# Optimization experiments

Hardware: AMD Instinct MI355X
Metric: run time of the kernel (lower is better)

## Reference

```python
import jax, jax.numpy as jnp
import numpy as np

N_NODES = 50000
N_EDGES = 1600000
IN_DIM, HIDDEN, OUT_DIM = 128, 128, 64


def setup_inputs() -> dict:
    key = jax.random.key(0)
    ks = jax.random.split(key, 8)
    x = jax.random.normal(ks[0], (N_NODES, IN_DIM), dtype=jnp.float32)
    edge_index = jax.random.randint(ks[1], (2, N_EDGES), 0, N_NODES, dtype=jnp.int64)
    # SAGEConv params: lin_l applied to aggregated neighbors (with bias),
    # lin_r applied to root/self features (no bias) -- PyG defaults.
    def lin_init(k, fan_in, fan_out):
        bound = 1.0 / np.sqrt(fan_in)
        return jax.random.uniform(k, (fan_in, fan_out), jnp.float32, -bound, bound)
    W1_l = lin_init(ks[2], IN_DIM, HIDDEN)
    W1_r = lin_init(ks[3], IN_DIM, HIDDEN)
    b1 = jnp.zeros((HIDDEN,), jnp.float32)
    W2_l = lin_init(ks[4], HIDDEN, OUT_DIM)
    W2_r = lin_init(ks[5], HIDDEN, OUT_DIM)
    b2 = jnp.zeros((OUT_DIM,), jnp.float32)
    return {"x": x, "edge_index": edge_index, "W1_l": W1_l, "W1_r": W1_r,
            "b1": b1, "W2_l": W2_l, "W2_r": W2_r, "b2": b2}


def _sage_conv(h, src, dst, n_nodes, W_l, W_r, b):
    # gather messages from source nodes, mean-aggregate at destinations
    msg = h[src]                                              # [E, D]
    agg_sum = jax.ops.segment_sum(msg, dst, num_segments=n_nodes)
    deg = jax.ops.segment_sum(jnp.ones((src.shape[0],), h.dtype), dst,
                              num_segments=n_nodes)
    agg_mean = agg_sum / jnp.maximum(deg, 1.0)[:, None]       # [N, D]
    return agg_mean @ W_l + h @ W_r + b


def reference(x, edge_index, W1_l, W1_r, b1, W2_l, W2_r, b2):
    n = x.shape[0]
    src, dst = edge_index[0], edge_index[1]
    h = jax.nn.relu(_sage_conv(x, src, dst, n, W1_l, W1_r, b1))
    return _sage_conv(h, src, dst, n, W2_l, W2_r, b2)
```

## Files before the change

kernel.cpp:

```cpp
#include <hip/hip_runtime.h>

#define NN 50000
#define NE 1600000
#define BSTRIDE 96
#define C_BKT 196
#define P1_BLKS 512
#define P1_CHUNK 3125
#define CAP 56
#define XCVT_BLKS 1563
#define WCVT_BLKS 48
#define PP_PREP (XCVT_BLKS + WCVT_BLKS)

typedef __bf16 bf16x8 __attribute__((ext_vector_type(8)));
typedef float  f32x4  __attribute__((ext_vector_type(4)));
typedef float  f32x2  __attribute__((ext_vector_type(2)));

__device__ __forceinline__ float bfLo(uint u) { union { uint i; float f; } v; v.i = u << 16; return v.f; }
__device__ __forceinline__ float bfHi(uint u) { union { uint i; float f; } v; v.i = u & 0xffff0000u; return v.f; }
__device__ __forceinline__ float bf1(ushort s) { union { uint i; float f; } v; v.i = (uint)s << 16; return v.f; }
__device__ __forceinline__ ushort f2bf(float f) {
    union { float f; uint i; } v; v.f = f;
    uint r = v.i + 0x7fffu + ((v.i >> 16) & 1u);
    return (ushort)(r >> 16);
}
__device__ __forceinline__ uint pack2(float a, float b) {
    return (uint)f2bf(a) | ((uint)f2bf(b) << 16);
}
__device__ __forceinline__ bf16x8 load8(const ushort* p) {
    union { uint4 u; bf16x8 b; } v; v.u = *(const uint4*)p; return v.b;
}

#define ACC8(u) { a0 += bfLo(u.x); a1 += bfHi(u.x); a2 += bfLo(u.y); a3 += bfHi(u.y); \
                  a4 += bfLo(u.z); a5 += bfHi(u.z); a6 += bfLo(u.w); a7 += bfHi(u.w); }

#define CVA(u, o) { f32x2 p0 = __builtin_amdgcn_cvt_pk_f32_fp8((int)(u), 0); \
                    f32x2 p1 = __builtin_amdgcn_cvt_pk_f32_fp8((int)(u), 1); \
                    a[(o)+0] += p0.x; a[(o)+1] += p0.y; a[(o)+2] += p1.x; a[(o)+3] += p1.y; }
#define ACCF8(v) { CVA((v).x, 0); CVA((v).y, 4); CVA((v).z, 8); CVA((v).w, 12); }

__global__ __launch_bounds__(1024) void k_pp(
    const float4* __restrict__ x, ushort4* __restrict__ xb, uint* __restrict__ xf8,
    const float* __restrict__ W1l, const float* __restrict__ W1r,
    const float* __restrict__ W2l, const float* __restrict__ W2r,
    ushort* __restrict__ T1l, ushort* __restrict__ T1r,
    ushort* __restrict__ T2l, ushort* __restrict__ T2r,
    const int* __restrict__ src, const int* __restrict__ dst,
    uint* __restrict__ cells, ushort* __restrict__ cnt) {
    __shared__ uint hist[C_BKT];
    const int b = blockIdx.x;
    const int tid = threadIdx.x;
    if (b < XCVT_BLKS) {
        int i = b * 1024 + tid;
        if (i < NN * 128 / 4) {
            float4 v = x[i];
            ushort4 o; o.x = f2bf(v.x); o.y = f2bf(v.y); o.z = f2bf(v.z); o.w = f2bf(v.w);
            xb[i] = o;
            uint r = (uint)__builtin_amdgcn_cvt_pk_fp8_f32(v.x, v.y, 0, 0);
            r = (uint)__builtin_amdgcn_cvt_pk_fp8_f32(v.z, v.w, (int)r, 1);
            xf8[i] = r;
        }
    } else if (b < PP_PREP) {
        int i = (b - XCVT_BLKS) * 1024 + tid;
        if (i < 16384) {
            int k = i >> 7, n = i & 127; T1l[n * 128 + k] = f2bf(W1l[i]);
        } else if (i < 32768) {
            int j = i - 16384; int k = j >> 7, n = j & 127; T1r[n * 128 + k] = f2bf(W1r[j]);
        } else if (i < 40960) {
            int j = i - 32768; int k = j >> 6, n = j & 63;  T2l[n * 128 + k] = f2bf(W2l[j]);
        } else {
            int j = i - 40960; int k = j >> 6, n = j & 63;  T2r[n * 128 + k] = f2bf(W2r[j]);
        }
    } else {
        const int b2 = b - PP_PREP;
        for (int i = tid; i < C_BKT; i += 1024) hist[i] = 0;
        __syncthreads();
        const int beg = b2 * P1_CHUNK;
        uint* myCells = cells + (size_t)b2 * C_BKT * CAP;
        for (int i = beg + tid; i < beg + P1_CHUNK; i += 1024) {
            int d = dst[i];
            int s = src[i];
            int c = d >> 8;
            uint p = atomicAdd(&hist[c], 1);
            if (p < CAP) myCells[c * CAP + p] = ((uint)(d & 255) << 16) | (uint)s;
        }
        __syncthreads();
        for (int i = tid; i < C_BKT; i += 1024)
            cnt[(size_t)b2 * C_BKT + i] = (ushort)min(hist[i], (uint)CAP);
    }
}

__global__ __launch_bounds__(1024) void k_part2(const uint* __restrict__ cells,
                        const ushort* __restrict__ cnt,
                        ushort* __restrict__ col, int* __restrict__ deg) {
    __shared__ uint hist[256];
    const int c = blockIdx.x;
    if (threadIdx.x < 256) hist[threadIdx.x] = 0;
    __syncthreads();
    const int b = threadIdx.x >> 1;
    const int sub = threadIdx.x & 1;
    const uint* cell = cells + ((size_t)b * C_BKT + c) * CAP;
    const int n = cnt[(size_t)b * C_BKT + c];
    const int nodeBase = c << 8;
    for (int j = sub; j < n; j += 2) {
        uint e = cell[j];
        int dl = e >> 16;
        uint p = atomicAdd(&hist[dl], 1);
        if (p < BSTRIDE)
            col[(size_t)(nodeBase + dl) * BSTRIDE + p] = (ushort)(e & 0xFFFF);
    }
    __syncthreads();
    if (threadIdx.x < 256) {
        int node = nodeBase + threadIdx.x;
        if (node < NN) deg[node] = (int)hist[threadIdx.x];
    }
}

__global__ void k_agg128(const uchar* __restrict__ xf8, const ushort* __restrict__ col,
                         const int* __restrict__ deg, ushort* __restrict__ out) {
    int node = (blockIdx.x * blockDim.x + threadIdx.x) >> 6;
    int lane = threadIdx.x & 63;
    int q = lane >> 3;
    int c = lane & 7;
    int d = deg[node];
    int dd = min(d, BSTRIDE);
    const ushort* cb = col + (size_t)node * BSTRIDE;
    float a[16];
    #pragma unroll
    for (int i = 0; i < 16; i++) a[i] = 0.f;
    for (int j0 = 0; j0 < dd; j0 += 64) {
        int idx = (j0 + lane < dd) ? (int)cb[j0 + lane] : 0;
        int cnt = min(64, dd - j0);
        int t = 0;
        for (; t + 16 <= cnt; t += 16) {
            int s0 = __shfl(idx, t + q);
            int s1 = __shfl(idx, t + 8 + q);
            uint4 u0 = *(const uint4*)(xf8 + (size_t)s0 * 128 + c * 16);
            uint4 u1 = *(const uint4*)(xf8 + (size_t)s1 * 128 + c * 16);
            ACCF8(u0); ACCF8(u1);
        }
        for (; t < cnt; t += 8) {
            int s = __shfl(idx, t + q);
            if (t + q < cnt) {
                uint4 u = *(const uint4*)(xf8 + (size_t)s * 128 + c * 16);
                ACCF8(u);
            }
        }
    }
    #pragma unroll
    for (int m = 8; m < 64; m <<= 1) {
        #pragma unroll
        for (int i = 0; i < 16; i++) a[i] += __shfl_xor(a[i], m);
    }
    if (q == 0) {
        float inv = 1.f / fmaxf((float)d, 1.f);
        uint4 o;
        o.x = pack2(a[0] * inv, a[1] * inv);
        o.y = pack2(a[2] * inv, a[3] * inv);
        o.z = pack2(a[4] * inv, a[5] * inv);
        o.w = pack2(a[6] * inv, a[7] * inv);
        *(uint4*)(out + (size_t)node * 128 + c * 16) = o;
        o.x = pack2(a[8] * inv, a[9] * inv);
        o.y = pack2(a[10] * inv, a[11] * inv);
        o.z = pack2(a[12] * inv, a[13] * inv);
        o.w = pack2(a[14] * inv, a[15] * inv);
        *(uint4*)(out + (size_t)node * 128 + c * 16 + 8) = o;
    }
}

__global__ void k_agg64(const ushort* __restrict__ feat, const ushort* __restrict__ col,
                        const int* __restrict__ deg, ushort* __restrict__ out) {
    int node = (blockIdx.x * blockDim.x + threadIdx.x) >> 6;
    int lane = threadIdx.x & 63;
    int q = lane >> 3;
    int c = lane & 7;
    int d = deg[node];
    int dd = min(d, BSTRIDE);
    const ushort* cb = col + (size_t)node * BSTRIDE;
    float a0=0.f,a1=0.f,a2=0.f,a3=0.f,a4=0.f,a5=0.f,a6=0.f,a7=0.f;
    for (int j0 = 0; j0 < dd; j0 += 64) {
        int idx = (j0 + lane < dd) ? (int)cb[j0 + lane] : 0;
        int cnt = min(64, dd - j0);
        int t = 0;
        for (; t + 16 <= cnt; t += 16) {
            int s0 = __shfl(idx, t + q);
            int s1 = __shfl(idx, t + 8 + q);
            uint4 u0 = *(const uint4*)(feat + (size_t)s0 * 128 + c * 8);
            uint4 u1 = *(const uint4*)(feat + (size_t)s1 * 128 + c * 8);
            ACC8(u0); ACC8(u1);
        }
        for (; t < cnt; t += 8) {
            int s = __shfl(idx, t + q);
            if (t + q < cnt) {
                uint4 u = *(const uint4*)(feat + (size_t)s * 128 + c * 8);
                ACC8(u);
            }
        }
    }
    #pragma unroll
    for (int m = 8; m < 64; m <<= 1) {
        a0 += __shfl_xor(a0, m); a1 += __shfl_xor(a1, m);
        a2 += __shfl_xor(a2, m); a3 += __shfl_xor(a3, m);
        a4 += __shfl_xor(a4, m); a5 += __shfl_xor(a5, m);
        a6 += __shfl_xor(a6, m); a7 += __shfl_xor(a7, m);
    }
    if (q == 0) {
        float inv = 1.f / fmaxf((float)d, 1.f);
        uint4 o;
        o.x = pack2(a0 * inv, a1 * inv);
        o.y = pack2(a2 * inv, a3 * inv);
        o.z = pack2(a4 * inv, a5 * inv);
        o.w = pack2(a6 * inv, a7 * inv);
        *(uint4*)(out + (size_t)node * 128 + c * 8) = o;
    }
}

#define PAD1 136
__global__ __launch_bounds__(256) void k_gemm12(
    const ushort* __restrict__ agg, const ushort* __restrict__ xb,
    const ushort* __restrict__ T1l, const ushort* __restrict__ T1r,
    const ushort* __restrict__ T2l, const float* __restrict__ bias,
    ushort* __restrict__ h, ushort* __restrict__ hW) {
    __shared__ ushort hS[2][16 * PAD1];
    const int lane = threadIdx.x & 63;
    const int wave = threadIdx.x >> 6;
    const int s = wave >> 1;
    const int ch = wave & 1;
    const int quad = lane >> 4, r16 = lane & 15;
    const int row0 = blockIdx.x * 32 + s * 16;
    const int arow = min(row0 + r16, NN - 1);
    ushort* myS = &hS[s][0];
    f32x4 acc[4];
    #pragma unroll
    for (int nt = 0; nt < 4; nt++) acc[nt] = (f32x4){0.f, 0.f, 0.f, 0.f};

    #pragma unroll
    for (int kt = 0; kt < 4; kt++) {
        const int k = kt * 32 + quad * 8;
        bf16x8 aAgg = load8(agg + (size_t)arow * 128 + k);
        bf16x8 aXb  = load8(xb + (size_t)arow * 128 + k);
        #pragma unroll
        for (int nt = 0; nt < 4; nt++) {
            const int wr = ch * 64 + nt * 16 + r16;
            acc[nt] = __builtin_amdgcn_mfma_f32_16x16x32_bf16(aAgg, load8(T1l + wr * 128 + k), acc[nt], 0, 0, 0);
            acc[nt] = __builtin_amdgcn_mfma_f32_16x16x32_bf16(aXb,  load8(T1r + wr * 128 + k), acc[nt], 0, 0, 0);
        }
    }
    #pragma unroll
    for (int nt = 0; nt < 4; nt++) {
        int cc = ch * 64 + nt * 16 + r16;
        float bv = bias[cc];
        #pragma unroll
        for (int i = 0; i < 4; i++) {
            int lr = quad * 4 + i;
            int rr = row0 + lr;
            ushort val = f2bf(fmaxf(acc[nt][i] + bv, 0.f));
            myS[lr * PAD1 + cc] = val;
            if (rr < NN) h[(size_t)rr * 128 + cc] = val;
        }
    }
    __syncthreads();
    f32x4 acc2[2];
    #pragma unroll
    for (int nt = 0; nt < 2; nt++) acc2[nt] = (f32x4){0.f, 0.f, 0.f, 0.f};
    #pragma unroll
    for (int kt = 0; kt < 4; kt++) {
        const int k = kt * 32 + quad * 8;
        bf16x8 ah = load8(&myS[r16 * PAD1 + k]);
        #pragma unroll
        for (int nt = 0; nt < 2; nt++) {
            const int wr = ch * 32 + nt * 16 + r16;
            acc2[nt] = __builtin_amdgcn_mfma_f32_16x16x32_bf16(ah, load8(T2l + wr * 128 + k), acc2[nt], 0, 0, 0);
        }
    }
    #pragma unroll
    for (int nt = 0; nt < 2; nt++) {
        int cc = ch * 32 + nt * 16 + r16;
        #pragma unroll
        for (int i = 0; i < 4; i++) {
            int rr = row0 + quad * 4 + i;
            if (rr < NN) hW[(size_t)rr * 128 + cc] = f2bf(acc2[nt][i]);
        }
    }
}

__global__ __launch_bounds__(256) void k_gemm2b(
    const ushort* __restrict__ A, const ushort* __restrict__ WT,
    const ushort* __restrict__ addend, const float* __restrict__ bias,
    float* __restrict__ out) {
    const int lane = threadIdx.x & 63;
    const int wave = threadIdx.x >> 6;
    const int s = wave >> 1, ch = wave & 1;
    const int quad = lane >> 4, r16 = lane & 15;
    const int row0 = blockIdx.x * 32 + s * 16;
    const int arow = min(row0 + r16, NN - 1);
    f32x4 acc[2];
    #pragma unroll
    for (int nt = 0; nt < 2; nt++) acc[nt] = (f32x4){0.f, 0.f, 0.f, 0.f};
    #pragma unroll
    for (int kt = 0; kt < 4; kt++) {
        const int k = kt * 32 + quad * 8;
        bf16x8 af = load8(A + (size_t)arow * 128 + k);
        #pragma unroll
        for (int nt = 0; nt < 2; nt++) {
            const int wr = ch * 32 + nt * 16 + r16;
            acc[nt] = __builtin_amdgcn_mfma_f32_16x16x32_bf16(af, load8(WT + wr * 128 + k), acc[nt], 0, 0, 0);
        }
    }
    #pragma unroll
    for (int nt = 0; nt < 2; nt++) {
        int cc = ch * 32 + nt * 16 + r16;
        #pragma unroll
        for (int i = 0; i < 4; i++) {
            int rr = row0 + quad * 4 + i;
            if (rr < NN)
                out[(size_t)rr * 64 + cc] = acc[nt][i] + bf1(addend[(size_t)rr * 128 + cc]) + bias[cc];
        }
    }
}

extern "C" void kernel_launch(void* const* d_in, const int* in_sizes, int n_in,
                              void* d_out, int out_size, void* d_ws, size_t ws_size,
                              hipStream_t stream) {
    const float* x   = (const float*)d_in[0];
    const int*   ei  = (const int*)d_in[1];
    const float* W1l = (const float*)d_in[2];
    const float* W1r = (const float*)d_in[3];
    const float* b1  = (const float*)d_in[4];
    const float* W2l = (const float*)d_in[5];
    const float* W2r = (const float*)d_in[6];
    const float* b2  = (const float*)d_in[7];
    float* out = (float*)d_out;

    const int* src = ei;
    const int* dst = ei + NE;

    char* w = (char*)d_ws;
    ushort* col   = (ushort*)w;                  w += (size_t)NN * BSTRIDE * 2;
    int* deg      = (int*)w;                     w += (size_t)50048 * 4;
    ushort* cnt   = (ushort*)w;                  w += (size_t)P1_BLKS * C_BKT * 2;
    ushort* xb    = (ushort*)w;                  w += (size_t)NN * 128 * 2;
    ushort* T1l   = (ushort*)w;                  w += 128 * 128 * 2;
    ushort* T1r   = (ushort*)w;                  w += 128 * 128 * 2;
    ushort* T2l   = (ushort*)w;                  w += 64 * 128 * 2;
    ushort* T2r   = (ushort*)w;                  w += 64 * 128 * 2;
    ushort* aggR  = (ushort*)w;                  w += (size_t)NN * 128 * 2;
    ushort* h     = (ushort*)w;                  w += (size_t)NN * 128 * 2;
    uchar* xf8    = (uchar*)w;                   w += (size_t)NN * 128;
    ushort* agg1 = aggR;
    ushort* hW   = aggR;
    ushort* agg2 = aggR + 64;
    uint* cells  = (uint*)aggR;

    k_pp<<<PP_PREP + P1_BLKS, 1024, 0, stream>>>(
        (const float4*)x, (ushort4*)xb, (uint*)xf8, W1l, W1r, W2l, W2r,
        T1l, T1r, T2l, T2r, src, dst, cells, cnt);
    k_part2<<<C_BKT, 1024, 0, stream>>>(cells, cnt, col, deg);

    k_agg128<<<NN / 4, 256, 0, stream>>>(xf8, col, deg, agg1);
    k_gemm12<<<(NN + 31) / 32, 256, 0, stream>>>(agg1, xb, T1l, T1r, T2l, b1, h, hW);

    k_agg64<<<NN / 4, 256, 0, stream>>>(hW, col, deg, agg2);
    k_gemm2b<<<(NN + 31) / 32, 256, 0, stream>>>(h, T2r, agg2, b2, out);
}
```

Measured before the change: 236.4 us.

## Fuse layer-2 root GEMM into layer-1 GEMM and add it in aggregation epilogue

Layer-1 GEMM now also computes h@W2_r+b2 into an fp32 buffer, so h is never written to global memory. The final aggregation kernel adds that partial directly to the mean-aggregated result, which removes the separate k_gemm2b launch. hW is now stored compactly with a 64-element row stride instead of 128, which shrinks the gather footprint. A-operand loads are hoisted ahead of the MFMA loops. In exchange an fp32 intermediate of N×64 is written and read back.

```diff
diff --git a/kernel.cpp b/kernel.cpp
--- a/kernel.cpp
+++ b/kernel.cpp
@@ -167,8 +167,95 @@
     }
 }
 
-__global__ void k_agg64(const ushort* __restrict__ feat, const ushort* __restrict__ col,
-                        const int* __restrict__ deg, ushort* __restrict__ out) {
+#define PAD1 136
+__global__ __launch_bounds__(256) void k_gemm12(
+    const ushort* __restrict__ agg, const ushort* __restrict__ xb,
+    const ushort* __restrict__ T1l, const ushort* __restrict__ T1r,
+    const ushort* __restrict__ T2l, const ushort* __restrict__ T2r,
+    const float* __restrict__ b1, const float* __restrict__ b2,
+    ushort* __restrict__ hW, float* __restrict__ outp) {
+    __shared__ ushort hS[2][16 * PAD1];
+    const int lane = threadIdx.x & 63;
+    const int wave = threadIdx.x >> 6;
+    const int s = wave >> 1;
+    const int ch = wave & 1;
+    const int quad = lane >> 4, r16 = lane & 15;
+    const int row0 = blockIdx.x * 32 + s * 16;
+    const int arow = min(row0 + r16, NN - 1);
+    ushort* myS = &hS[s][0];
+
+    bf16x8 aAgg[4], aXb[4];
+    #pragma unroll
+    for (int kt = 0; kt < 4; kt++) {
+        const int k = kt * 32 + quad * 8;
+        aAgg[kt] = load8(agg + (size_t)arow * 128 + k);
+        aXb[kt]  = load8(xb  + (size_t)arow * 128 + k);
+    }
+
+    f32x4 acc[4];
+    #pragma unroll
+    for (int nt = 0; nt < 4; nt++) acc[nt] = (f32x4){0.f, 0.f, 0.f, 0.f};
+    #pragma unroll
+    for (int kt = 0; kt < 4; kt++) {
+        const int k = kt * 32 + quad * 8;
+        #pragma unroll
+        for (int nt = 0; nt < 4; nt++) {
+            const int wr = ch * 64 + nt * 16 + r16;
+            acc[nt] = __builtin_amdgcn_mfma_f32_16x16x32_bf16(aAgg[kt], load8(T1l + wr * 128 + k), acc[nt], 0, 0, 0);
+            acc[nt] = __builtin_amdgcn_mfma_f32_16x16x32_bf16(aXb[kt],  load8(T1r + wr * 128 + k), acc[nt], 0, 0, 0);
+        }
+    }
+    #pragma unroll
+    for (int nt = 0; nt < 4; nt++) {
+        int cc = ch * 64 + nt * 16 + r16;
+        float bv = b1[cc];
+        #pragma unroll
+        for (int i = 0; i < 4; i++) {
+            int lr = quad * 4 + i;
+            myS[lr * PAD1 + cc] = f2bf(fmaxf(acc[nt][i] + bv, 0.f));
+        }
+    }
+    __syncthreads();
+
+    bf16x8 ah[4];
+    #pragma unroll
+    for (int kt = 0; kt < 4; kt++)
+        ah[kt] = load8(&myS[r16 * PAD1 + kt * 32 + quad * 8]);
+
+    f32x4 acc2[2], acc3[2];
+    #pragma unroll
+    for (int nt = 0; nt < 2; nt++) {
+        acc2[nt] = (f32x4){0.f, 0.f, 0.f, 0.f};
+        acc3[nt] = (f32x4){0.f, 0.f, 0.f, 0.f};
+    }
+    #pragma unroll
+    for (int kt = 0; kt < 4; kt++) {
+        const int k = kt * 32 + quad * 8;
+        #pragma unroll
+        for (int nt = 0; nt < 2; nt++) {
+            const int wr = ch * 32 + nt * 16 + r16;
+            acc2[nt] = __builtin_amdgcn_mfma_f32_16x16x32_bf16(ah[kt], load8(T2l + wr * 128 + k), acc2[nt], 0, 0, 0);
+            acc3[nt] = __builtin_amdgcn_mfma_f32_16x16x32_bf16(ah[kt], load8(T2r + wr * 128 + k), acc3[nt], 0, 0, 0);
+        }
+    }
+    #pragma unroll
+    for (int nt = 0; nt < 2; nt++) {
+        int cc = ch * 32 + nt * 16 + r16;
+        float bv = b2[cc];
+        #pragma unroll
+        for (int i = 0; i < 4; i++) {
+            int rr = row0 + quad * 4 + i;
+            if (rr < NN) {
+                hW[(size_t)rr * 64 + cc] = f2bf(acc2[nt][i]);
+                outp[(size_t)rr * 64 + cc] = acc3[nt][i] + bv;
+            }
+        }
+    }
+}
+
+__global__ void k_agg64f(const ushort* __restrict__ hW, const ushort* __restrict__ col,
+                         const int* __restrict__ deg, const float* __restrict__ outp,
+                         float* __restrict__ out) {
     int node = (blockIdx.x * blockDim.x + threadIdx.x) >> 6;
     int lane = threadIdx.x & 63;
     int q = lane >> 3;
@@ -184,14 +271,14 @@
         for (; t + 16 <= cnt; t += 16) {
             int s0 = __shfl(idx, t + q);
             int s1 = __shfl(idx, t + 8 + q);
-            uint4 u0 = *(const uint4*)(feat + (size_t)s0 * 128 + c * 8);
-            uint4 u1 = *(const uint4*)(feat + (size_t)s1 * 128 + c * 8);
+            uint4 u0 = *(const uint4*)(hW + (size_t)s0 * 64 + c * 8);
+            uint4 u1 = *(const uint4*)(hW + (size_t)s1 * 64 + c * 8);
             ACC8(u0); ACC8(u1);
         }
         for (; t < cnt; t += 8) {
             int s = __shfl(idx, t + q);
             if (t + q < cnt) {
-                uint4 u = *(const uint4*)(feat + (size_t)s * 128 + c * 8);
+                uint4 u = *(const uint4*)(hW + (size_t)s * 64 + c * 8);
                 ACC8(u);
             }
         }
@@ -205,116 +292,15 @@
     }
     if (q == 0) {
         float inv = 1.f / fmaxf((float)d, 1.f);
-        uint4 o;
-        o.x = pack2(a0 * inv, a1 * inv);
-        o.y = pack2(a2 * inv, a3 * inv);
-        o.z = pack2(a4 * inv, a5 * inv);
-        o.w = pack2(a6 * inv, a7 * inv);
-        *(uint4*)(out + (size_t)node * 128 + c * 8) = o;
-    }
-}
-
-#define PAD1 136
-__global__ __launch_bounds__(256) void k_gemm12(
-    const ushort* __restrict__ agg, const ushort* __restrict__ xb,
-    const ushort* __restrict__ T1l, const ushort* __restrict__ T1r,
-    const ushort* __restrict__ T2l, const float* __restrict__ bias,
-    ushort* __restrict__ h, ushort* __restrict__ hW) {
-    __shared__ ushort hS[2][16 * PAD1];
-    const int lane = threadIdx.x & 63;
-    const int wave = threadIdx.x >> 6;
-    const int s = wave >> 1;
-    const int ch = wave & 1;
-    const int quad = lane >> 4, r16 = lane & 15;
-    const int row0 = blockIdx.x * 32 + s * 16;
-    const int arow = min(row0 + r16, NN - 1);
-    ushort* myS = &hS[s][0];
-    f32x4 acc[4];
-    #pragma unroll
-    for (int nt = 0; nt < 4; nt++) acc[nt] = (f32x4){0.f, 0.f, 0.f, 0.f};
-
-    #pragma unroll
-    for (int kt = 0; kt < 4; kt++) {
-        const int k = kt * 32 + quad * 8;
-        bf16x8 aAgg = load8(agg + (size_t)arow * 128 + k);
-        bf16x8 aXb  = load8(xb + (size_t)arow * 128 + k);
-        #pragma unroll
-        for (int nt = 0; nt < 4; nt++) {
-            const int wr = ch * 64 + nt * 16 + r16;
-            acc[nt] = __builtin_amdgcn_mfma_f32_16x16x32_bf16(aAgg, load8(T1l + wr * 128 + k), acc[nt], 0, 0, 0);
-            acc[nt] = __builtin_amdgcn_mfma_f32_16x16x32_bf16(aXb,  load8(T1r + wr * 128 + k), acc[nt], 0, 0, 0);
-        }
-    }
-    #pragma unroll
-    for (int nt = 0; nt < 4; nt++) {
-        int cc = ch * 64 + nt * 16 + r16;
-        float bv = bias[cc];
-        #pragma unroll
-        for (int i = 0; i < 4; i++) {
-            int lr = quad * 4 + i;
-            int rr = row0 + lr;
-            ushort val = f2bf(fmaxf(acc[nt][i] + bv, 0.f));
-            myS[lr * PAD1 + cc] = val;
-            if (rr < NN) h[(size_t)rr * 128 + cc] = val;
-        }
-    }
-    __syncthreads();
-    f32x4 acc2[2];
-    #pragma unroll
-    for (int nt = 0; nt < 2; nt++) acc2[nt] = (f32x4){0.f, 0.f, 0.f, 0.f};
-    #pragma unroll
-    for (int kt = 0; kt < 4; kt++) {
-        const int k = kt * 32 + quad * 8;
-        bf16x8 ah = load8(&myS[r16 * PAD1 + k]);
-        #pragma unroll
-        for (int nt = 0; nt < 2; nt++) {
-            const int wr = ch * 32 + nt * 16 + r16;
-            acc2[nt] = __builtin_amdgcn_mfma_f32_16x16x32_bf16(ah, load8(T2l + wr * 128 + k), acc2[nt], 0, 0, 0);
-        }
-    }
-    #pragma unroll
-    for (int nt = 0; nt < 2; nt++) {
-        int cc = ch * 32 + nt * 16 + r16;
-        #pragma unroll
-        for (int i = 0; i < 4; i++) {
-            int rr = row0 + quad * 4 + i;
-            if (rr < NN) hW[(size_t)rr * 128 + cc] = f2bf(acc2[nt][i]);
-        }
-    }
-}
-
-__global__ __launch_bounds__(256) void k_gemm2b(
-    const ushort* __restrict__ A, const ushort* __restrict__ WT,
-    const ushort* __restrict__ addend, const float* __restrict__ bias,
-    float* __restrict__ out) {
-    const int lane = threadIdx.x & 63;
-    const int wave = threadIdx.x >> 6;
-    const int s = wave >> 1, ch = wave & 1;
-    const int quad = lane >> 4, r16 = lane & 15;
-    const int row0 = blockIdx.x * 32 + s * 16;
-    const int arow = min(row0 + r16, NN - 1);
-    f32x4 acc[2];
-    #pragma unroll
-    for (int nt = 0; nt < 2; nt++) acc[nt] = (f32x4){0.f, 0.f, 0.f, 0.f};
-    #pragma unroll
-    for (int kt = 0; kt < 4; kt++) {
-        const int k = kt * 32 + quad * 8;
-        bf16x8 af = load8(A + (size_t)arow * 128 + k);
-        #pragma unroll
-        for (int nt = 0; nt < 2; nt++) {
-            const int wr = ch * 32 + nt * 16 + r16;
-            acc[nt] = __builtin_amdgcn_mfma_f32_16x16x32_bf16(af, load8(WT + wr * 128 + k), acc[nt], 0, 0, 0);
-        }
-    }
-    #pragma unroll
-    for (int nt = 0; nt < 2; nt++) {
-        int cc = ch * 32 + nt * 16 + r16;
-        #pragma unroll
-        for (int i = 0; i < 4; i++) {
-            int rr = row0 + quad * 4 + i;
-            if (rr < NN)
-                out[(size_t)rr * 64 + cc] = acc[nt][i] + bf1(addend[(size_t)rr * 128 + cc]) + bias[cc];
-        }
+        float4 p0 = *(const float4*)(outp + (size_t)node * 64 + c * 8);
+        float4 p1 = *(const float4*)(outp + (size_t)node * 64 + c * 8 + 4);
+        float4 o;
+        o.x = a0 * inv + p0.x; o.y = a1 * inv + p0.y;
+        o.z = a2 * inv + p0.z; o.w = a3 * inv + p0.w;
+        *(float4*)(out + (size_t)node * 64 + c * 8) = o;
+        o.x = a4 * inv + p1.x; o.y = a5 * inv + p1.y;
+        o.z = a6 * inv + p1.z; o.w = a7 * inv + p1.w;
+        *(float4*)(out + (size_t)node * 64 + c * 8 + 4) = o;
     }
 }
 
@@ -343,13 +329,11 @@
     ushort* T1r   = (ushort*)w;                  w += 128 * 128 * 2;
     ushort* T2l   = (ushort*)w;                  w += 64 * 128 * 2;
     ushort* T2r   = (ushort*)w;                  w += 64 * 128 * 2;
-    ushort* aggR  = (ushort*)w;                  w += (size_t)NN * 128 * 2;
-    ushort* h     = (ushort*)w;                  w += (size_t)NN * 128 * 2;
+    ushort* agg1  = (ushort*)w;                  w += (size_t)NN * 128 * 2;
+    ushort* hW    = (ushort*)w;                  w += (size_t)NN * 64 * 2;
+    float* outp   = (float*)w;                   w += (size_t)NN * 64 * 4;
     uchar* xf8    = (uchar*)w;                   w += (size_t)NN * 128;
-    ushort* agg1 = aggR;
-    ushort* hW   = aggR;
-    ushort* agg2 = aggR + 64;
-    uint* cells  = (uint*)aggR;
+    uint* cells  = (uint*)agg1;
 
     k_pp<<<PP_PREP + P1_BLKS, 1024, 0, stream>>>(
         (const float4*)x, (ushort4*)xb, (uint*)xf8, W1l, W1r, W2l, W2r,
@@ -357,8 +341,7 @@
     k_part2<<<C_BKT, 1024, 0, stream>>>(cells, cnt, col, deg);
 
     k_agg128<<<NN / 4, 256, 0, stream>>>(xf8, col, deg, agg1);
-    k_gemm12<<<(NN + 31) / 32, 256, 0, stream>>>(agg1, xb, T1l, T1r, T2l, b1, h, hW);
-
-    k_agg64<<<NN / 4, 256, 0, stream>>>(hW, col, deg, agg2);
-    k_gemm2b<<<(NN + 31) / 32, 256, 0, stream>>>(h, T2r, agg2, b2, out);
-}
+    k_gemm12<<<(NN + 31) / 32, 256, 0, stream>>>(agg1, xb, T1l, T1r, T2l, T2r, b1, b2, hW, outp);
+
+    k_agg64f<<<NN / 4, 256, 0, stream>>>(hW, col, deg, outp, out);
+}
```

After: 221.8 us. -6.2%, faster.
